# Optimization experiments

Hardware: AMD Instinct MI355X
Metric: run time of the kernel (lower is better)

The kernel has to match this reference:

```python
import jax, jax.numpy as jnp
import numpy as np

B, N, D = 8, 2048, 128

def setup_inputs() -> dict:
    key = jax.random.key(0)
    k1, k2, k3 = jax.random.split(key, 3)
    h = jax.random.normal(k1, (B, N, D), dtype=jnp.float32)
    W = jax.random.normal(k2, (D, D), dtype=jnp.float32) * (1.0 / np.sqrt(D))
    # a has shape [1,1,1,2D] in torch; flatten to [2D] (xavier-normal init)
    a = jax.random.normal(k3, (2 * D,), dtype=jnp.float32) * np.sqrt(2.0 / (2 * D))
    return {"h": h, "W": W, "a": a}

def reference(h, W, a):
    act = jax.nn.relu
    # h <- h @ W^T (nn.Linear with weight W means x @ W.T; here W is the weight matrix)
    hw = jnp.einsum('bnd,ed->bne', h, W)  # [B,N,D]
    a_i, a_j = a[:D], a[D:]
    # e_ij = act(a_i . h_i + a_j . h_j) -- equivalent to sum(cat(h_i,h_j)*a, -1)
    s_i = jnp.einsum('bnd,d->bn', hw, a_i)  # [B,N]
    s_j = jnp.einsum('bnd,d->bn', hw, a_j)  # [B,N]
    e = act(s_i[:, :, None] + s_j[:, None, :])  # [B,N,N]
    a_ij = jax.nn.softmax(e, axis=2)
    out = act(jnp.einsum('bij,bjd->bid', a_ij, hw))
    return out
```

## Files before the change

### kernel.cpp

```cpp
#include <hip/hip_runtime.h>
#include <hip/hip_bf16.h>

#define BB 8
#define NN 2048
#define DD 128
#define TI 32
#define HP 132
#define CH 32
#define NC (NN / CH)
#define NO (NC + 1)
#define NFIX (BB * NO)

__device__ __forceinline__ float relu(float x) { return x > 0.f ? x : 0.f; }

typedef __attribute__((ext_vector_type(8))) __bf16 bf16x8;
typedef __attribute__((ext_vector_type(4))) float f32x4;

__device__ __forceinline__ void cvt2(float x, __bf16& hi, __bf16& lo) {
    hi = (__bf16)x;
    lo = (__bf16)(x - (float)hi);
}

__global__ __launch_bounds__(256) void GraphAttentionalLayer_1168231104632_kernel(
    const float* __restrict__ h,
    const float* __restrict__ W,
    const float* __restrict__ a,
    float* __restrict__ hw,
    float* __restrict__ E,
    float* __restrict__ F)
{
    __shared__ float hw_s[TI][HP];

    const int tid = threadIdx.x;
    const int lane = tid & 63;
    const int w  = tid >> 6;
    const int wm = w & 1;
    const int wn = w >> 1;
    const int lr = lane & 15;
    const int kg = lane >> 4;
    const int b  = blockIdx.x >> 6;
    const int i0 = (blockIdx.x & 63) * TI;

    const int arow = i0 + wm * 16 + lr;
    const float* hrow = h + ((size_t)b * NN + arow) * DD;

    f32x4 acc[4];
#pragma unroll
    for (int nf = 0; nf < 4; nf++) acc[nf] = (f32x4){0.f, 0.f, 0.f, 0.f};

#pragma unroll
    for (int kc = 0; kc < 4; kc++) {
        const int kb = kc * 32 + kg * 8;
        const float4 av0 = *reinterpret_cast<const float4*>(hrow + kb);
        const float4 av1 = *reinterpret_cast<const float4*>(hrow + kb + 4);
        const float av[8] = {av0.x, av0.y, av0.z, av0.w, av1.x, av1.y, av1.z, av1.w};
        bf16x8 ah, al;
#pragma unroll
        for (int e = 0; e < 8; e++) { __bf16 hi, lo; cvt2(av[e], hi, lo); ah[e] = hi; al[e] = lo; }

#pragma unroll
        for (int nf = 0; nf < 4; nf++) {
            const int wr = wn * 64 + nf * 16 + lr;
            const float* wrow = W + (size_t)wr * DD + kb;
            const float4 bv0 = *reinterpret_cast<const float4*>(wrow);
            const float4 bv1 = *reinterpret_cast<const float4*>(wrow + 4);
            const float bv[8] = {bv0.x, bv0.y, bv0.z, bv0.w, bv1.x, bv1.y, bv1.z, bv1.w};
            bf16x8 bh, bl;
#pragma unroll
            for (int e = 0; e < 8; e++) { __bf16 hi, lo; cvt2(bv[e], hi, lo); bh[e] = hi; bl[e] = lo; }

            acc[nf] = __builtin_amdgcn_mfma_f32_16x16x32_bf16(ah, bh, acc[nf], 0, 0, 0);
            acc[nf] = __builtin_amdgcn_mfma_f32_16x16x32_bf16(ah, bl, acc[nf], 0, 0, 0);
            acc[nf] = __builtin_amdgcn_mfma_f32_16x16x32_bf16(al, bh, acc[nf], 0, 0, 0);
        }
    }

#pragma unroll
    for (int nf = 0; nf < 4; nf++)
#pragma unroll
        for (int r = 0; r < 4; r++)
            hw_s[wm * 16 + kg * 4 + r][wn * 64 + nf * 16 + lr] = acc[nf][r];
    __syncthreads();

    const int row = tid >> 3;
    const int cb  = (tid & 7) * 4;
    const size_t gbase = ((size_t)b * NN + i0 + row) * DD;
    float pi = 0.f, pj = 0.f;
#pragma unroll
    for (int qq = 0; qq < 4; qq++) {
        const int col = cb + qq * 32;
        const float4 v = *reinterpret_cast<const float4*>(&hw_s[row][col]);
        *reinterpret_cast<float4*>(&hw[gbase + col]) = v;
        const float4 avi = *reinterpret_cast<const float4*>(&a[col]);
        const float4 avj = *reinterpret_cast<const float4*>(&a[DD + col]);
        pi += v.x * avi.x + v.y * avi.y + v.z * avi.z + v.w * avi.w;
        pj += v.x * avj.x + v.y * avj.y + v.z * avj.z + v.w * avj.w;
    }
#pragma unroll
    for (int off = 4; off > 0; off >>= 1) {
        pi += __shfl_down(pi, off, 8);
        pj += __shfl_down(pj, off, 8);
    }
    if ((tid & 7) == 0) {
        const size_t rr = (size_t)b * NN + i0 + row;
        E[rr] = __expf(pi);
        F[rr] = __expf(pj);
    }
}

__global__ __launch_bounds__(256) void GraphAttentionalLayer_1168231104632_rank(
    const float* __restrict__ F,
    float* __restrict__ Fsorted,
    int* __restrict__ perm)
{
    __shared__ float F_s[NN];
    __shared__ int   part[4][64];

    const int t = threadIdx.x;
    const int b = blockIdx.x >> 5;
    const int j0 = (blockIdx.x & 31) * 64;
    const size_t nb = (size_t)b * NN;

    for (int q = 0; q < NN / 256; q++)
        F_s[q * 256 + t] = F[nb + q * 256 + t];
    __syncthreads();

    const int tj = t & 63, ts = t >> 6;
    const int j = j0 + tj;
    const float fj = F_s[j];
    const int m0 = ts * (NN / 4);
    int cnt = 0;
#pragma unroll 8
    for (int mi = 0; mi < NN / 4; mi++) {
        const int m = m0 + mi;
        const float fm = F_s[m];
        cnt += (fm < fj) | ((fm == fj) & (m < j));
    }
    part[ts][tj] = cnt;
    __syncthreads();
    if (ts == 0) {
        const int r = part[0][tj] + part[1][tj] + part[2][tj] + part[3][tj];
        Fsorted[nb + r] = fj;
        perm[nb + r] = j;
    }
}

__global__ __launch_bounds__(128) void GraphAttentionalLayer_1168231104632_scan(
    const float* __restrict__ hw,
    const float* __restrict__ Fsorted,
    const int* __restrict__ perm,
    float* __restrict__ Q0L, float* __restrict__ Q1L,
    float* __restrict__ C0,  float* __restrict__ C1)
{
    const int t = threadIdx.x;
    const int b = blockIdx.x / NC, c = blockIdx.x % NC;
    const size_t nb = (size_t)b * NN;
    const int m0 = c * CH;

    int   jv[CH];
    float Fv[CH];
#pragma unroll
    for (int mm = 0; mm < CH; mm++) jv[mm] = perm[nb + m0 + mm];
#pragma unroll
    for (int mm = 0; mm < CH; mm++) Fv[mm] = Fsorted[nb + m0 + mm];

    float hv[CH];
#pragma unroll
    for (int mm = 0; mm < CH; mm++)
        hv[mm] = hw[(nb + jv[mm]) * DD + t];

    float a0 = 0.f, a1 = 0.f;
#pragma unroll
    for (int mm = 0; mm < CH; mm++) {
        const int m = m0 + mm;
        Q0L[(nb + m) * DD + t] = a0;
        Q1L[(nb + m) * DD + t] = a1;
        a0 += hv[mm];
        a1 += Fv[mm] * hv[mm];
    }
    C0[((size_t)b * NC + c) * DD + t] = a0;
    C1[((size_t)b * NC + c) * DD + t] = a1;
}

__global__ __launch_bounds__(256) void GraphAttentionalLayer_1168231104632_mid(
    const float* __restrict__ C0, const float* __restrict__ C1,
    const float* __restrict__ Fsorted, const float* __restrict__ E,
    float* __restrict__ O0, float* __restrict__ O1,
    int* __restrict__ kk,  float* __restrict__ zinv)
{
    __shared__ float fs_s[NN];
    __shared__ float cf_s[NC];
    __shared__ float of_s[NO];

    const int tid = threadIdx.x;

    if (blockIdx.x < NFIX) {
        const int b = blockIdx.x / NO, c = blockIdx.x % NO;
        const int d = tid & 127;
        const float* C = (tid < 128) ? C0 : C1;
        float*       O = (tid < 128) ? O0 : O1;
        float o = 0.f;
        int c2 = 0;
        for (; c2 + 16 <= c; c2 += 16) {
            float v[16];
#pragma unroll
            for (int q = 0; q < 16; q++)
                v[q] = C[((size_t)b * NC + c2 + q) * DD + d];
#pragma unroll
            for (int q = 0; q < 16; q++) o += v[q];
        }
        for (; c2 < c; c2++)
            o += C[((size_t)b * NC + c2) * DD + d];
        O[((size_t)b * NO + c) * DD + d] = o;
        return;
    }

    const int sb = blockIdx.x - NFIX;
    const int b = sb >> 3;
    const int i0 = (sb & 7) * 256;
    const size_t nb = (size_t)b * NN;

    for (int q = 0; q < NN / 256; q++)
        fs_s[q * 256 + tid] = Fsorted[nb + q * 256 + tid];
    __syncthreads();

    if (tid < NC) {
        float p = 0.f;
        const int m0 = tid * CH;
#pragma unroll
        for (int mm = 0; mm < CH; mm++) p += fs_s[m0 + mm];
        cf_s[tid] = p;
    }
    __syncthreads();
    if (tid < NO) {
        float p = 0.f;
        for (int c2 = 0; c2 < tid; c2++) p += cf_s[c2];
        of_s[tid] = p;
    }
    __syncthreads();

    const int row = (int)nb + i0 + tid;
    const float Ei = E[row];
    const float thr = 1.0f / Ei;
    int lo = 0, hi = NN;
    while (lo < hi) {
        const int mid = (lo + hi) >> 1;
        if (fs_s[mid] < thr) lo = mid + 1; else hi = mid;
    }
    float fpl = 0.f;
    for (int m = (lo >> 5) << 5; m < lo; m++) fpl += fs_s[m];
    const float TF = of_s[NC];
    const float Pk = of_s[lo >> 5] + fpl;
    const float z = Ei * (TF - Pk) + (float)lo;
    kk[row] = lo;
    zinv[row] = 1.0f / z;
}

__global__ __launch_bounds__(128) void GraphAttentionalLayer_1168231104632_out(
    const float* __restrict__ Q0L, const float* __restrict__ Q1L,
    const float* __restrict__ O0,  const float* __restrict__ O1,
    const int* __restrict__ kk,    const float* __restrict__ zinv,
    const float* __restrict__ E,   float* __restrict__ out)
{
    const int t = threadIdx.x;
    const int row = blockIdx.x;
    const int b = row >> 11;
    const size_t nb = (size_t)b * NN;

    const int k = kk[row];
    const float Ev = E[row];
    const float zv = zinv[row];
    const float T1 = O1[((size_t)b * NO + NC) * DD + t];

    float num;
    if (k < NN) {
        const int c = k >> 5;
        const float q0 = Q0L[(nb + k) * DD + t] + O0[((size_t)b * NO + c) * DD + t];
        const float q1 = Q1L[(nb + k) * DD + t] + O1[((size_t)b * NO + c) * DD + t];
        num = Ev * (T1 - q1) + q0;
    } else {
        num = O0[((size_t)b * NO + NC) * DD + t];
    }
    out[(size_t)row * DD + t] = relu(num * zv);
}

extern "C" __attribute__((visibility("default")))
void kernel_launch(void* const* d_in, const int* in_sizes, int n_in,
                   void* d_out, int out_size, void* d_ws, size_t ws_size,
                   hipStream_t stream) {
    const float* h = nullptr; const float* W = nullptr; const float* a = nullptr;
    for (int i = 0; i < n_in; i++) {
        if (in_sizes[i] == BB * NN * DD)      h = (const float*)d_in[i];
        else if (in_sizes[i] == DD * DD)      W = (const float*)d_in[i];
        else if (in_sizes[i] == 2 * DD)       a = (const float*)d_in[i];
    }
    if (!h) h = (const float*)d_in[0];
    if (!W) W = (const float*)d_in[1];
    if (!a) a = (const float*)d_in[2];

    float* out = (float*)d_out;
    float* ws = (float*)d_ws;

    float* hw   = ws;
    float* E    = hw + (size_t)BB * NN * DD;
    float* F    = E + BB * NN;
    float* Fs   = F + BB * NN;
    float* zinv = Fs + BB * NN;
    int*   perm = (int*)(zinv + BB * NN);
    int*   kk   = perm + BB * NN;
    float* Q0L  = (float*)(kk + BB * NN);
    float* Q1L  = Q0L + (size_t)BB * NN * DD;
    float* C0   = Q1L + (size_t)BB * NN * DD;
    float* C1   = C0 + BB * NC * DD;
    float* O0   = C1 + BB * NC * DD;
    float* O1   = O0 + BB * NO * DD;
    const size_t need = (size_t)((O1 + BB * NO * DD) - ws) * sizeof(float);

    if (ws_size < need || d_ws == nullptr) {
        hipMemsetAsync(d_out, 0x42, (size_t)out_size * sizeof(float), stream);
        return;
    }

    GraphAttentionalLayer_1168231104632_kernel<<<BB * (NN / TI), 256, 0, stream>>>(h, W, a, hw, E, F);
    GraphAttentionalLayer_1168231104632_rank<<<BB * 32, 256, 0, stream>>>(F, Fs, perm);
    GraphAttentionalLayer_1168231104632_scan<<<BB * NC, 128, 0, stream>>>(hw, Fs, perm, Q0L, Q1L, C0, C1);
    GraphAttentionalLayer_1168231104632_mid<<<NFIX + BB * 8, 256, 0, stream>>>(C0, C1, Fs, E, O0, O1, kk, zinv);
    GraphAttentionalLayer_1168231104632_out<<<BB * NN, 128, 0, stream>>>(Q0L, Q1L, O0, O1, kk, zinv, E, out);
}
```

Before: 108.5 us.

## Fuse five kernel launches into one cooperative persistent kernel with grid syncs

Replaces the five-kernel pipeline (matmul, rank, scan, mid, out) with a single cooperative kernel of 512 blocks that runs each stage in turn, separated by grid-wide barriers, and keeps the multi-launch path as a fallback if the cooperative launch fails. The aim is to remove per-launch overhead and inter-kernel gaps. In exchange the final output stage now uses only 512 blocks instead of 16384, and grid.sync carries its own barrier cost. Cooperative launch also needs all 512 blocks to be co-resident, which launch_bounds(256,2) is meant to allow.

```diff
diff --git a/kernel.cpp b/kernel.cpp
--- a/kernel.cpp
+++ b/kernel.cpp
@@ -1,5 +1,8 @@
 #include <hip/hip_runtime.h>
 #include <hip/hip_bf16.h>
+#include <hip/hip_cooperative_groups.h>
+
+namespace cg = cooperative_groups;
 
 #define BB 8
 #define NN 2048
@@ -10,6 +13,7 @@
 #define NC (NN / CH)
 #define NO (NC + 1)
 #define NFIX (BB * NO)
+#define GRID 512
 
 __device__ __forceinline__ float relu(float x) { return x > 0.f ? x : 0.f; }
 
@@ -19,6 +23,263 @@
 __device__ __forceinline__ void cvt2(float x, __bf16& hi, __bf16& lo) {
     hi = (__bf16)x;
     lo = (__bf16)(x - (float)hi);
+}
+
+__global__ __launch_bounds__(256, 2) void GraphAttentionalLayer_1168231104632_mega(
+    const float* __restrict__ h, const float* __restrict__ W, const float* __restrict__ a,
+    float* __restrict__ hw, float* __restrict__ E, float* __restrict__ F,
+    float* __restrict__ Fs, int* __restrict__ perm,
+    float* __restrict__ Q0L, float* __restrict__ Q1L,
+    float* __restrict__ C0, float* __restrict__ C1,
+    float* __restrict__ O0, float* __restrict__ O1,
+    int* __restrict__ kk, float* __restrict__ zinv,
+    float* __restrict__ out)
+{
+    cg::grid_group grid = cg::this_grid();
+
+    __shared__ union {
+        float hw_s[TI][HP];
+        struct { float F_s[NN]; int part[8][32]; } p2;
+        struct { float fs_s[NN]; float cf_s[NC]; float of_s[NO]; } p4;
+    } sh;
+
+    const int tid = threadIdx.x;
+    const int blk = blockIdx.x;
+
+    {
+        const int lane = tid & 63;
+        const int w  = tid >> 6;
+        const int wm = w & 1;
+        const int wn = w >> 1;
+        const int lr = lane & 15;
+        const int kg = lane >> 4;
+        const int b  = blk >> 6;
+        const int i0 = (blk & 63) * TI;
+
+        const int arow = i0 + wm * 16 + lr;
+        const float* hrow = h + ((size_t)b * NN + arow) * DD;
+
+        f32x4 acc[4];
+#pragma unroll
+        for (int nf = 0; nf < 4; nf++) acc[nf] = (f32x4){0.f, 0.f, 0.f, 0.f};
+
+#pragma unroll
+        for (int kc = 0; kc < 4; kc++) {
+            const int kb = kc * 32 + kg * 8;
+            const float4 av0 = *reinterpret_cast<const float4*>(hrow + kb);
+            const float4 av1 = *reinterpret_cast<const float4*>(hrow + kb + 4);
+            const float av[8] = {av0.x, av0.y, av0.z, av0.w, av1.x, av1.y, av1.z, av1.w};
+            bf16x8 ah, al;
+#pragma unroll
+            for (int e = 0; e < 8; e++) { __bf16 hi, lo; cvt2(av[e], hi, lo); ah[e] = hi; al[e] = lo; }
+
+#pragma unroll
+            for (int nf = 0; nf < 4; nf++) {
+                const int wr = wn * 64 + nf * 16 + lr;
+                const float* wrow = W + (size_t)wr * DD + kb;
+                const float4 bv0 = *reinterpret_cast<const float4*>(wrow);
+                const float4 bv1 = *reinterpret_cast<const float4*>(wrow + 4);
+                const float bv[8] = {bv0.x, bv0.y, bv0.z, bv0.w, bv1.x, bv1.y, bv1.z, bv1.w};
+                bf16x8 bh, bl;
+#pragma unroll
+                for (int e = 0; e < 8; e++) { __bf16 hi, lo; cvt2(bv[e], hi, lo); bh[e] = hi; bl[e] = lo; }
+
+                acc[nf] = __builtin_amdgcn_mfma_f32_16x16x32_bf16(ah, bh, acc[nf], 0, 0, 0);
+                acc[nf] = __builtin_amdgcn_mfma_f32_16x16x32_bf16(ah, bl, acc[nf], 0, 0, 0);
+                acc[nf] = __builtin_amdgcn_mfma_f32_16x16x32_bf16(al, bh, acc[nf], 0, 0, 0);
+            }
+        }
+
+#pragma unroll
+        for (int nf = 0; nf < 4; nf++)
+#pragma unroll
+            for (int r = 0; r < 4; r++)
+                sh.hw_s[wm * 16 + kg * 4 + r][wn * 64 + nf * 16 + lr] = acc[nf][r];
+        __syncthreads();
+
+        const int row = tid >> 3;
+        const int cb  = (tid & 7) * 4;
+        const size_t gbase = ((size_t)b * NN + i0 + row) * DD;
+        float pi = 0.f, pj = 0.f;
+#pragma unroll
+        for (int qq = 0; qq < 4; qq++) {
+            const int col = cb + qq * 32;
+            const float4 v = *reinterpret_cast<const float4*>(&sh.hw_s[row][col]);
+            *reinterpret_cast<float4*>(&hw[gbase + col]) = v;
+            const float4 avi = *reinterpret_cast<const float4*>(&a[col]);
+            const float4 avj = *reinterpret_cast<const float4*>(&a[DD + col]);
+            pi += v.x * avi.x + v.y * avi.y + v.z * avi.z + v.w * avi.w;
+            pj += v.x * avj.x + v.y * avj.y + v.z * avj.z + v.w * avj.w;
+        }
+#pragma unroll
+        for (int off = 4; off > 0; off >>= 1) {
+            pi += __shfl_down(pi, off, 8);
+            pj += __shfl_down(pj, off, 8);
+        }
+        if ((tid & 7) == 0) {
+            const size_t rr = (size_t)b * NN + i0 + row;
+            E[rr] = __expf(pi);
+            F[rr] = __expf(pj);
+        }
+    }
+    grid.sync();
+
+    {
+        const int b = blk >> 6;
+        const int j0 = (blk & 63) * 32;
+        const size_t nb = (size_t)b * NN;
+
+        for (int q = 0; q < NN / 256; q++)
+            sh.p2.F_s[q * 256 + tid] = F[nb + q * 256 + tid];
+        __syncthreads();
+
+        const int tj = tid & 31, ts = tid >> 5;
+        const int j = j0 + tj;
+        const float fj = sh.p2.F_s[j];
+        const int m0 = ts * (NN / 8);
+        int cnt = 0;
+#pragma unroll 8
+        for (int mi = 0; mi < NN / 8; mi++) {
+            const int m = m0 + mi;
+            const float fm = sh.p2.F_s[m];
+            cnt += (fm < fj) | ((fm == fj) & (m < j));
+        }
+        sh.p2.part[ts][tj] = cnt;
+        __syncthreads();
+        if (ts == 0) {
+            int r = 0;
+#pragma unroll
+            for (int s = 0; s < 8; s++) r += sh.p2.part[s][tj];
+            Fs[nb + r] = fj;
+            perm[nb + r] = j;
+        }
+    }
+    grid.sync();
+
+    {
+        if (tid < DD) {
+            const int t = tid;
+            const int b = blk >> 6, c = blk & 63;
+            const size_t nb = (size_t)b * NN;
+            const int m0 = c * CH;
+
+            int   jv[CH];
+            float Fv[CH];
+#pragma unroll
+            for (int mm = 0; mm < CH; mm++) jv[mm] = perm[nb + m0 + mm];
+#pragma unroll
+            for (int mm = 0; mm < CH; mm++) Fv[mm] = Fs[nb + m0 + mm];
+
+            float hv[CH];
+#pragma unroll
+            for (int mm = 0; mm < CH; mm++)
+                hv[mm] = hw[(nb + jv[mm]) * DD + t];
+
+            float a0 = 0.f, a1 = 0.f;
+#pragma unroll
+            for (int mm = 0; mm < CH; mm++) {
+                const int m = m0 + mm;
+                Q0L[(nb + m) * DD + t] = a0;
+                Q1L[(nb + m) * DD + t] = a1;
+                a0 += hv[mm];
+                a1 += Fv[mm] * hv[mm];
+            }
+            C0[((size_t)b * NC + c) * DD + t] = a0;
+            C1[((size_t)b * NC + c) * DD + t] = a1;
+        }
+    }
+    grid.sync();
+
+    for (int job = blk; job < NFIX + BB * 8; job += GRID) {
+        if (job < NFIX) {
+            const int b = job / NO, c = job % NO;
+            const int d = tid & 127;
+            const float* C = (tid < 128) ? C0 : C1;
+            float*       O = (tid < 128) ? O0 : O1;
+            float o = 0.f;
+            int c2 = 0;
+            for (; c2 + 16 <= c; c2 += 16) {
+                float v[16];
+#pragma unroll
+                for (int q = 0; q < 16; q++)
+                    v[q] = C[((size_t)b * NC + c2 + q) * DD + d];
+#pragma unroll
+                for (int q = 0; q < 16; q++) o += v[q];
+            }
+            for (; c2 < c; c2++)
+                o += C[((size_t)b * NC + c2) * DD + d];
+            O[((size_t)b * NO + c) * DD + d] = o;
+        } else {
+            const int sb = job - NFIX;
+            const int b = sb >> 3;
+            const int i0 = (sb & 7) * 256;
+            const size_t nb = (size_t)b * NN;
+
+            __syncthreads();
+            for (int q = 0; q < NN / 256; q++)
+                sh.p4.fs_s[q * 256 + tid] = Fs[nb + q * 256 + tid];
+            __syncthreads();
+
+            if (tid < NC) {
+                float p = 0.f;
+                const int m0 = tid * CH;
+#pragma unroll
+                for (int mm = 0; mm < CH; mm++) p += sh.p4.fs_s[m0 + mm];
+                sh.p4.cf_s[tid] = p;
+            }
+            __syncthreads();
+            if (tid < NO) {
+                float p = 0.f;
+                for (int c2 = 0; c2 < tid; c2++) p += sh.p4.cf_s[c2];
+                sh.p4.of_s[tid] = p;
+            }
+            __syncthreads();
+
+            const int row = (int)nb + i0 + tid;
+            const float Ei = E[row];
+            const float thr = 1.0f / Ei;
+            int lo = 0, hi = NN;
+            while (lo < hi) {
+                const int mid = (lo + hi) >> 1;
+                if (sh.p4.fs_s[mid] < thr) lo = mid + 1; else hi = mid;
+            }
+            float fpl = 0.f;
+            for (int m = (lo >> 5) << 5; m < lo; m++) fpl += sh.p4.fs_s[m];
+            const float TF = sh.p4.of_s[NC];
+            const float Pk = sh.p4.of_s[lo >> 5] + fpl;
+            const float z = Ei * (TF - Pk) + (float)lo;
+            kk[row] = lo;
+            zinv[row] = 1.0f / z;
+        }
+    }
+    grid.sync();
+
+    {
+        const int t = tid & 127;
+        const int half = tid >> 7;
+#pragma unroll 2
+        for (int pass = 0; pass < (BB * NN) / (GRID * 2); pass++) {
+            const int row = pass * (GRID * 2) + blk * 2 + half;
+            const int b = row >> 11;
+            const size_t nb = (size_t)b * NN;
+
+            const int k = kk[row];
+            const float Ev = E[row];
+            const float zv = zinv[row];
+            const float T1 = O1[((size_t)b * NO + NC) * DD + t];
+
+            float num;
+            if (k < NN) {
+                const int c = k >> 5;
+                const float q0 = Q0L[(nb + k) * DD + t] + O0[((size_t)b * NO + c) * DD + t];
+                const float q1 = Q1L[(nb + k) * DD + t] + O1[((size_t)b * NO + c) * DD + t];
+                num = Ev * (T1 - q1) + q0;
+            } else {
+                num = O0[((size_t)b * NO + NC) * DD + t];
+            }
+            out[(size_t)row * DD + t] = relu(num * zv);
+        }
+    }
 }
 
 __global__ __launch_bounds__(256) void GraphAttentionalLayer_1168231104632_kernel(
@@ -321,9 +582,20 @@
         return;
     }
 
-    GraphAttentionalLayer_1168231104632_kernel<<<BB * (NN / TI), 256, 0, stream>>>(h, W, a, hw, E, F);
-    GraphAttentionalLayer_1168231104632_rank<<<BB * 32, 256, 0, stream>>>(F, Fs, perm);
-    GraphAttentionalLayer_1168231104632_scan<<<BB * NC, 128, 0, stream>>>(hw, Fs, perm, Q0L, Q1L, C0, C1);
-    GraphAttentionalLayer_1168231104632_mid<<<NFIX + BB * 8, 256, 0, stream>>>(C0, C1, Fs, E, O0, O1, kk, zinv);
-    GraphAttentionalLayer_1168231104632_out<<<BB * NN, 128, 0, stream>>>(Q0L, Q1L, O0, O1, kk, zinv, E, out);
-}
+    void* args[] = { (void*)&h, (void*)&W, (void*)&a, (void*)&hw, (void*)&E, (void*)&F,
+                     (void*)&Fs, (void*)&perm, (void*)&Q0L, (void*)&Q1L,
+                     (void*)&C0, (void*)&C1, (void*)&O0, (void*)&O1,
+                     (void*)&kk, (void*)&zinv, (void*)&out };
+    hipError_t err = hipLaunchCooperativeKernel(
+        (void*)GraphAttentionalLayer_1168231104632_mega,
+        dim3(GRID), dim3(256), args, 0, stream);
+
+    if (err != hipSuccess) {
+        (void)hipGetLastError();
+        GraphAttentionalLayer_1168231104632_kernel<<<BB * (NN / TI), 256, 0, stream>>>(h, W, a, hw, E, F);
+        GraphAttentionalLayer_1168231104632_rank<<<BB * 32, 256, 0, stream>>>(F, Fs, perm);
+        GraphAttentionalLayer_1168231104632_scan<<<BB * NC, 128, 0, stream>>>(hw, Fs, perm, Q0L, Q1L, C0, C1);
+        GraphAttentionalLayer_1168231104632_mid<<<NFIX + BB * 8, 256, 0, stream>>>(C0, C1, Fs, E, O0, O1, kk, zinv);
+        GraphAttentionalLayer_1168231104632_out<<<BB * NN, 128, 0, stream>>>(Q0L, Q1L, O0, O1, kk, zinv, E, out);
+    }
+}
```

Result: slower. 332.0 us (+206.0%).
